# Kernel optimization log

Hardware: AMD Instinct MI355X
Metric: run time of the kernel (lower is better)

The kernel has to match this reference:

```python
import jax, jax.numpy as jnp
import numpy as np

QK_K = 256          # values per Q4_K super-block
TYPE_SIZE = 144     # bytes per Q4_K block: 2 (d fp16) + 2 (dmin fp16) + 12 (scales) + 128 (qs)
OUT_FEATURES = 8192
IN_FEATURES = 8192
BATCH = 256


def setup_inputs() -> dict:
    rng = np.random.default_rng(0)
    n_blocks = OUT_FEATURES * IN_FEATURES // QK_K
    # Pack valid little-endian fp16 super-block scales into raw bytes (as a GGUF file would store them).
    d16 = rng.uniform(0.001, 0.01, size=(n_blocks,)).astype(np.float16)
    dmin16 = rng.uniform(0.0005, 0.005, size=(n_blocks,)).astype(np.float16)
    scales = rng.integers(0, 256, size=(n_blocks, 12), dtype=np.uint8)  # packed 6-bit sub-scales/mins
    qs = rng.integers(0, 256, size=(n_blocks, 128), dtype=np.uint8)     # 4-bit quants, 2 per byte
    blocks = np.concatenate(
        [d16.view(np.uint8).reshape(n_blocks, 2),
         dmin16.view(np.uint8).reshape(n_blocks, 2),
         scales, qs], axis=1)  # [n_blocks, 144] uint8
    key = jax.random.key(0)
    kx, kb = jax.random.split(key)
    x = jax.random.normal(kx, (BATCH, IN_FEATURES), dtype=jnp.float32)
    bias = jax.random.normal(kb, (OUT_FEATURES,), dtype=jnp.float32) * 0.01
    return {"x": x, "qweight": jnp.asarray(blocks), "bias": bias}


def _bitcast_f16(bytes2):
    # bytes2: [n, 2] uint8 (little-endian) -> [n] float32
    n = bytes2.shape[0]
    return jax.lax.bitcast_convert_type(bytes2.reshape(n, 1, 2), jnp.float16).reshape(n).astype(jnp.float32)


def _get_scale_min(scales):
    # scales: [n, 12] uint8 -> 8 six-bit sub-block scales and mins, each [n, 8]
    n = scales.shape[0]
    s = scales.reshape(n, 3, 4)
    d_, m_, md = s[:, 0], s[:, 1], s[:, 2]  # each [n, 4]
    sc = jnp.concatenate([d_ & 63, (md & 15) | ((d_ >> 2) & 48)], axis=-1)
    mn = jnp.concatenate([m_ & 63, (md >> 4) | ((m_ >> 2) & 48)], axis=-1)
    return sc, mn


def dequantize_q4_k(blocks):
    # blocks: [n_blocks, 144] uint8 -> [n_blocks, 256] float32
    n = blocks.shape[0]
    d = _bitcast_f16(blocks[:, 0:2])       # [n]
    dmin = _bitcast_f16(blocks[:, 2:4])    # [n]
    sc, mn = _get_scale_min(blocks[:, 4:16])
    dl = (d[:, None] * sc.astype(jnp.float32)).reshape(n, 8, 1)   # per-sub-block scale
    ml = (dmin[:, None] * mn.astype(jnp.float32)).reshape(n, 8, 1)  # per-sub-block min
    qs = blocks[:, 16:].reshape(n, 4, 1, 32)                       # 128 bytes
    shift = jnp.array([0, 4], dtype=jnp.uint8).reshape(1, 1, 2, 1)
    q = ((qs >> shift) & 15).reshape(n, 8, 32).astype(jnp.float32)  # low then high nibbles
    return (dl * q - ml).reshape(n, QK_K)


def reference(x, qweight, bias):
    qweight = qweight.astype(jnp.uint8)
    W = dequantize_q4_k(qweight).reshape(OUT_FEATURES, IN_FEATURES)  # [out, in]
    return x @ W.T + bias  # F.linear(x, W, bias)
```

## Files before the change

### kernel.cpp

```cpp
#include <hip/hip_runtime.h>
#include <hip/hip_fp16.h>

typedef __bf16 bf16x8 __attribute__((ext_vector_type(8)));
typedef float floatx16 __attribute__((ext_vector_type(16)));
typedef unsigned int uint;
typedef unsigned short ushort;
typedef uint  uintx4  __attribute__((ext_vector_type(4)));
typedef float floatx4 __attribute__((ext_vector_type(4)));

constexpr int Mdim = 256, Ndim = 8192, Kdim = 8192;
constexpr int BN = 64, KSPLIT = 4;
constexpr int KS = Kdim / KSPLIT;
constexpr int NT = KS / 64;
constexpr int KB = Kdim / 256;

union U8 { uint u[4]; bf16x8 v; };

__device__ __forceinline__ uint cvtpk(float lo, float hi) {
  uint r; asm("v_cvt_pk_bf16_f32 %0, %1, %2" : "=v"(r) : "v"(lo), "v"(hi));
  return r;
}

template <typename T>
__device__ __forceinline__ T gld(const void* p) {
  return *(const __attribute__((address_space(1))) T*)p;
}

__device__ __forceinline__ int bswz(int row, int ch) {
  return row * 128 + ((ch ^ (row & 15)) << 3);
}

template<bool PRE>
__global__ __launch_bounds__(256, 2)
void q4k_gemm(const float* __restrict__ x, const bf16x8* __restrict__ xbf,
              const int* __restrict__ qw, const float* __restrict__ bias,
              float* __restrict__ out)
{
  __shared__ ushort Bb[2][BN * 128];

  const int tid = threadIdx.x;
  const int bid = blockIdx.x;
  const int l  = (bid & 7) * 64 + (bid >> 3);
  const int nb = l >> 2;
  const int ks = l & 3;
  const int n0 = nb * BN;
  const int ks8 = ks * (KS >> 8);

  const int sr = tid >> 2;
  const int sq = tid & 3;

  const int lane = tid & 63;
  const int wave = tid >> 6;
  const int mb0  = wave * 2;
  const int brow = lane & 31;
  const int bco  = lane >> 5;

  const int* bp0 = qw + (n0 + sr) * (KB * 144);
  const bf16x8* xA0 = PRE ? (xbf + ((mb0    ) * 512 + ks * 128) * 64 + lane) : nullptr;
  const bf16x8* xA1 = PRE ? (xbf + ((mb0 + 1) * 512 + ks * 128) * 64 + lane) : nullptr;

  uintx4 R[4][2];
  uintx4 Mdd[2], M0[2], M1[2], M2[2];
  U8 pqL, pqH;
  bf16x8 aA[8], aB[8];
  floatx16 acc00 = {}, acc01 = {}, acc10 = {}, acc11 = {};

  auto gloadB = [&](int s2, int rs) {
    const int* qp = bp0 + (ks8 + (s2 >> 2)) * 144 + 16 + (s2 & 3) * 32 + sq * 8;
    R[rs][0] = gld<uintx4>(qp);
    R[rs][1] = gld<uintx4>(qp + 4);
  };

  auto mload = [&](int sbrel, int ms) {
    const int* bp = bp0 + (ks8 + sbrel) * 144;
    Mdd[ms] = gld<uintx4>(bp);
    M0[ms]  = gld<uintx4>(bp + 4);
    M1[ms]  = gld<uintx4>(bp + 8);
    M2[ms]  = gld<uintx4>(bp + 12);
  };

  auto gloadA = [&](int t, bf16x8 (&A)[8]) {
    if constexpr (PRE) {
      const int f = t * 4 * 64;
      #pragma unroll
      for (int kk = 0; kk < 4; ++kk) {
        A[kk]     = gld<bf16x8>(xA0 + f + kk * 64);
        A[4 + kk] = gld<bf16x8>(xA1 + f + kk * 64);
      }
    } else {
      const int kg = ks * KS + t * 64 + bco * 8;
      #pragma unroll
      for (int kk = 0; kk < 4; ++kk) {
        const float* fA = x + (mb0 * 32 + brow) * Kdim + kg + kk * 16;
        const float* fB = x + ((mb0 + 1) * 32 + brow) * Kdim + kg + kk * 16;
        const floatx4 p0 = gld<floatx4>(fA), p1 = gld<floatx4>(fA + 4);
        const floatx4 q0 = gld<floatx4>(fB), q1 = gld<floatx4>(fB + 4);
        U8 ua, ub;
        ua.u[0] = cvtpk(p0.x, p0.y); ua.u[1] = cvtpk(p0.z, p0.w);
        ua.u[2] = cvtpk(p1.x, p1.y); ua.u[3] = cvtpk(p1.z, p1.w);
        ub.u[0] = cvtpk(q0.x, q0.y); ub.u[1] = cvtpk(q0.z, q0.w);
        ub.u[2] = cvtpk(q1.x, q1.y); ub.u[3] = cvtpk(q1.z, q1.w);
        A[kk] = ua.v; A[4 + kk] = ub.v;
      }
    }
  };

  auto dequant = [&](int c, int rs, int ms) {
    const uintx4 dd = Mdd[ms];
    const float d  = __half2float(__ushort_as_half((ushort)((dd.x & 255u) | ((dd.y & 255u) << 8))));
    const float dm = __half2float(__ushort_as_half((ushort)((dd.z & 255u) | ((dd.w & 255u) << 8))));
    const uintx4 s0 = M0[ms], s1 = M1[ms], s2 = M2[ms];
    uint scA, scB, mnA, mnB;
    if (c == 0)      { scA = s0.x & 63u; scB = s0.y & 63u; mnA = s1.x & 63u; mnB = s1.y & 63u; }
    else if (c == 1) { scA = s0.z & 63u; scB = s0.w & 63u; mnA = s1.z & 63u; mnB = s1.w & 63u; }
    else if (c == 2) {
      scA = (s2.x & 15u) | ((s0.x >> 2) & 48u); scB = (s2.y & 15u) | ((s0.y >> 2) & 48u);
      mnA = (s2.x >> 4)  | ((s1.x >> 2) & 48u); mnB = (s2.y >> 4)  | ((s1.y >> 2) & 48u);
    } else {
      scA = (s2.z & 15u) | ((s0.z >> 2) & 48u); scB = (s2.w & 15u) | ((s0.w >> 2) & 48u);
      mnA = (s2.z >> 4)  | ((s1.z >> 2) & 48u); mnB = (s2.w >> 4)  | ((s1.w >> 2) & 48u);
    }
    const float dlA = d * (float)scA, mlA = dm * (float)mnA;
    const float dlB = d * (float)scB, mlB = dm * (float)mnB;
    float wl[8], wh[8];
    #pragma unroll
    for (int h = 0; h < 2; ++h) {
      const uintx4 qv = R[rs][h];
      wl[h*4+0] = fmaf(dlA, (float)(qv.x & 15u), -mlA);
      wl[h*4+1] = fmaf(dlA, (float)(qv.y & 15u), -mlA);
      wl[h*4+2] = fmaf(dlA, (float)(qv.z & 15u), -mlA);
      wl[h*4+3] = fmaf(dlA, (float)(qv.w & 15u), -mlA);
      wh[h*4+0] = fmaf(dlB, (float)(qv.x >> 4), -mlB);
      wh[h*4+1] = fmaf(dlB, (float)(qv.y >> 4), -mlB);
      wh[h*4+2] = fmaf(dlB, (float)(qv.z >> 4), -mlB);
      wh[h*4+3] = fmaf(dlB, (float)(qv.w >> 4), -mlB);
    }
    #pragma unroll
    for (int p = 0; p < 4; ++p) {
      pqL.u[p] = cvtpk(wl[2*p], wl[2*p+1]);
      pqH.u[p] = cvtpk(wh[2*p], wh[2*p+1]);
    }
  };

  auto bwrite = [&](int bufi, int h) {
    *(bf16x8*)&Bb[bufi][bswz(sr, h * 8 + sq)]     = pqL.v;
    *(bf16x8*)&Bb[bufi][bswz(sr, h * 8 + 4 + sq)] = pqH.v;
  };

  auto mstep = [&](int bufi, int h, const bf16x8 (&A)[8]) {
    #pragma unroll
    for (int kk = 0; kk < 4; ++kk) {
      const bf16x8 bq0 = *(const bf16x8*)&Bb[bufi][bswz(brow,      h * 8 + kk * 2 + bco)];
      const bf16x8 bq1 = *(const bf16x8*)&Bb[bufi][bswz(brow + 32, h * 8 + kk * 2 + bco)];
      acc00 = __builtin_amdgcn_mfma_f32_32x32x16_bf16(A[kk],     bq0, acc00, 0, 0, 0);
      acc01 = __builtin_amdgcn_mfma_f32_32x32x16_bf16(A[kk],     bq1, acc01, 0, 0, 0);
      acc10 = __builtin_amdgcn_mfma_f32_32x32x16_bf16(A[4 + kk], bq0, acc10, 0, 0, 0);
      acc11 = __builtin_amdgcn_mfma_f32_32x32x16_bf16(A[4 + kk], bq1, acc11, 0, 0, 0);
    }
  };

  mload(0, 0); mload(1, 1);
  gloadB(0, 0); gloadB(1, 1); gloadB(2, 2); gloadB(3, 3);
  gloadA(0, aA); gloadA(1, aB);
  dequant(0, 0, 0); bwrite(0, 0);
  dequant(1, 1, 0); bwrite(0, 1);
  asm volatile("s_waitcnt lgkmcnt(0)" ::: "memory");
  __builtin_amdgcn_s_barrier();
  __builtin_amdgcn_sched_barrier(0);

  #define MLOADJ(j)                                                          \
    if ((j) == 1) { const int sb_ = B / 2 + 2; if (sb_ < 8) mload(sb_, 0); } \
    else if ((j) == 3) { const int sb_ = B / 2 + 3; if (sb_ < 8) mload(sb_, 1); }

  #define PH2(j) {                                                           \
    const int p_ = B + (j);                                                  \
    const int s1_ = 2 * p_ + 2, s2_ = 2 * p_ + 3;                            \
    if (s1_ < NT) { dequant((2*(j)+2)&3, (2*(j)+2)&3, (((j)+1)>>1)&1);       \
                    bwrite(((j)&1)^1, 0); }                                  \
    if (s2_ < NT) { dequant((2*(j)+3)&3, (2*(j)+3)&3, (((j)+1)>>1)&1);       \
                    bwrite(((j)&1)^1, 1); }                                  \
    if (s1_ + 2 < NT) gloadB(s1_ + 2, (2*(j)+4)&3);                          \
    if (s2_ + 2 < NT) gloadB(s2_ + 2, (2*(j)+5)&3);                          \
    MLOADJ(j)                                                                \
    __builtin_amdgcn_s_setprio(1);                                           \
    mstep((j)&1, 0, aA);                                                     \
    __builtin_amdgcn_s_setprio(0);                                           \
    if (s1_ < NT) gloadA(s1_, aA);                                           \
    __builtin_amdgcn_s_setprio(1);                                           \
    mstep((j)&1, 1, aB);                                                     \
    __builtin_amdgcn_s_setprio(0);                                           \
    if (s2_ < NT) gloadA(s2_, aB);                                           \
    asm volatile("s_waitcnt lgkmcnt(0)" ::: "memory");                       \
    __builtin_amdgcn_s_barrier();                                            \
    __builtin_amdgcn_sched_barrier(0);                                       \
  }

  for (int i = 0; i < 4; ++i) {
    const int B = i * 4;
    PH2(0) PH2(1) PH2(2) PH2(3)
  }
  #undef PH2
  #undef MLOADJ

  const int gn0 = n0 + (lane & 31);
  const int gn1 = gn0 + 32;
  const float bv0 = (ks == 0) ? bias[gn0] : 0.0f;
  const float bv1 = (ks == 0) ? bias[gn1] : 0.0f;
  const int mrow = wave * 64 + 4 * (lane >> 5);
  #pragma unroll
  for (int r = 0; r < 16; ++r) {
    const int m = mrow + (r & 3) + 8 * (r >> 2);
    atomicAdd(&out[m * Ndim + gn0], acc00[r] + bv0);
    atomicAdd(&out[m * Ndim + gn1], acc01[r] + bv1);
    atomicAdd(&out[(m + 32) * Ndim + gn0], acc10[r] + bv0);
    atomicAdd(&out[(m + 32) * Ndim + gn1], acc11[r] + bv1);
  }
}

template<bool DOCVT>
__global__ __launch_bounds__(256)
void prep(const float* __restrict__ x, uintx4* __restrict__ xb,
          floatx4* __restrict__ out)
{
  const int gid = blockIdx.x * 256 + threadIdx.x;
  out[gid * 2]     = floatx4{0.f, 0.f, 0.f, 0.f};
  out[gid * 2 + 1] = floatx4{0.f, 0.f, 0.f, 0.f};
  if (DOCVT) {
    const int lane = gid & 63;
    const int m = ((gid >> 15) * 32) + (lane & 31);
    const int k = (((gid >> 6) & 511) * 16) + (lane >> 5) * 8;
    const floatx4 f0 = gld<floatx4>(x + m * Kdim + k);
    const floatx4 f1 = gld<floatx4>(x + m * Kdim + k + 4);
    uintx4 st;
    st.x = cvtpk(f0.x, f0.y); st.y = cvtpk(f0.z, f0.w);
    st.z = cvtpk(f1.x, f1.y); st.w = cvtpk(f1.z, f1.w);
    xb[gid] = st;
  }
}

extern "C" void kernel_launch(void* const* d_in, const int* in_sizes, int n_in,
                              void* d_out, int out_size, void* d_ws, size_t ws_size,
                              hipStream_t stream) {
  (void)in_sizes; (void)n_in; (void)out_size;
  const float* x    = (const float*)d_in[0];
  const int*   qw   = (const int*)d_in[1];
  const float* bias = (const float*)d_in[2];
  float* out = (float*)d_out;

  const size_t need = (size_t)Mdim * Kdim * 2;
  if (ws_size >= need) {
    prep<true><<<1024, 256, 0, stream>>>(x, (uintx4*)d_ws, (floatx4*)out);
    q4k_gemm<true><<<512, 256, 0, stream>>>(x, (const bf16x8*)d_ws, qw, bias, out);
  } else {
    prep<false><<<1024, 256, 0, stream>>>(x, nullptr, (floatx4*)out);
    q4k_gemm<false><<<512, 256, 0, stream>>>(x, nullptr, qw, bias, out);
  }
}
```

Measured before the change: 70.92 us.

## Stage Q4_K quant bytes through LDS via direct global-to-LDS loads

```diff
diff --git a/kernel.cpp b/kernel.cpp
--- a/kernel.cpp
+++ b/kernel.cpp
@@ -26,9 +26,20 @@
   return *(const __attribute__((address_space(1))) T*)p;
 }
 
+__device__ __forceinline__ void glds16(const void* g, void* l) {
+  __builtin_amdgcn_global_load_lds(
+      (const __attribute__((address_space(1))) uint*)g,
+      (__attribute__((address_space(3))) uint*)l, 16, 0, 0);
+}
+
 __device__ __forceinline__ int bswz(int row, int ch) {
   return row * 128 + ((ch ^ (row & 15)) << 3);
 }
+
+#define WAITVM_(n) asm volatile("s_waitcnt vmcnt(" #n ")" ::: "memory")
+#define WAITVM(n) WAITVM_(n)
+#define NOWAIT ((void)0)
+#define S6(s) ((s) % 6)
 
 template<bool PRE>
 __global__ __launch_bounds__(256, 2)
@@ -36,6 +47,7 @@
               const int* __restrict__ qw, const float* __restrict__ bias,
               float* __restrict__ out)
 {
+  __shared__ __align__(16) int Qs[6 * 2048];
   __shared__ ushort Bb[2][BN * 128];
 
   const int tid = threadIdx.x;
@@ -59,16 +71,21 @@
   const bf16x8* xA0 = PRE ? (xbf + ((mb0    ) * 512 + ks * 128) * 64 + lane) : nullptr;
   const bf16x8* xA1 = PRE ? (xbf + ((mb0 + 1) * 512 + ks * 128) * 64 + lane) : nullptr;
 
-  uintx4 R[4][2];
   uintx4 Mdd[2], M0[2], M1[2], M2[2];
   U8 pqL, pqH;
   bf16x8 aA[8], aB[8];
   floatx16 acc00 = {}, acc01 = {}, acc10 = {}, acc11 = {};
 
-  auto gloadB = [&](int s2, int rs) {
-    const int* qp = bp0 + (ks8 + (s2 >> 2)) * 144 + 16 + (s2 & 3) * 32 + sq * 8;
-    R[rs][0] = gld<uintx4>(qp);
-    R[rs][1] = gld<uintx4>(qp + 4);
+  auto stageQ = [&](int s, int slot) {
+    const int sb = s >> 2, c64 = s & 3;
+    const int schk = ((lane & 7) ^ (lane >> 3)) << 2;
+    #pragma unroll
+    for (int j = 0; j < 2; ++j) {
+      const int r = j * 32 + wave * 8 + (lane >> 3);
+      const int* src = qw + (n0 + r) * (KB * 144) + (ks8 + sb) * 144
+                       + 16 + c64 * 32 + schk;
+      glds16((const void*)src, (void*)&Qs[slot * 2048 + (j * 256 + wave * 64) * 4]);
+    }
   };
 
   auto mload = [&](int sbrel, int ms) {
@@ -105,7 +122,10 @@
     }
   };
 
-  auto dequant = [&](int c, int rs, int ms) {
+  auto dequant = [&](int c, int slot, int ms) {
+    const int* qrow = &Qs[slot * 2048 + sr * 32];
+    const uintx4 q0 = *(const uintx4*)(qrow + ((( 2 * sq)     ^ (sr & 7)) << 2));
+    const uintx4 q1 = *(const uintx4*)(qrow + ((( 2 * sq + 1) ^ (sr & 7)) << 2));
     const uintx4 dd = Mdd[ms];
     const float d  = __half2float(__ushort_as_half((ushort)((dd.x & 255u) | ((dd.y & 255u) << 8))));
     const float dm = __half2float(__ushort_as_half((ushort)((dd.z & 255u) | ((dd.w & 255u) << 8))));
@@ -125,7 +145,7 @@
     float wl[8], wh[8];
     #pragma unroll
     for (int h = 0; h < 2; ++h) {
-      const uintx4 qv = R[rs][h];
+      const uintx4 qv = h ? q1 : q0;
       wl[h*4+0] = fmaf(dlA, (float)(qv.x & 15u), -mlA);
       wl[h*4+1] = fmaf(dlA, (float)(qv.y & 15u), -mlA);
       wl[h*4+2] = fmaf(dlA, (float)(qv.z & 15u), -mlA);
@@ -159,48 +179,53 @@
     }
   };
 
+  stageQ(0, 0); stageQ(1, 1);
+  stageQ(2, 2); stageQ(3, 3);
   mload(0, 0); mload(1, 1);
-  gloadB(0, 0); gloadB(1, 1); gloadB(2, 2); gloadB(3, 3);
   gloadA(0, aA); gloadA(1, aB);
+  stageQ(4, 4); stageQ(5, 5);
+  WAITVM(32);
+  __builtin_amdgcn_s_barrier();
   dequant(0, 0, 0); bwrite(0, 0);
   dequant(1, 1, 0); bwrite(0, 1);
+  WAITVM(28);
   asm volatile("s_waitcnt lgkmcnt(0)" ::: "memory");
   __builtin_amdgcn_s_barrier();
   __builtin_amdgcn_sched_barrier(0);
 
-  #define MLOADJ(j)                                                          \
-    if ((j) == 1) { const int sb_ = B / 2 + 2; if (sb_ < 8) mload(sb_, 0); } \
-    else if ((j) == 3) { const int sb_ = B / 2 + 3; if (sb_ < 8) mload(sb_, 1); }
-
-  #define PH2(j) {                                                           \
-    const int p_ = B + (j);                                                  \
-    const int s1_ = 2 * p_ + 2, s2_ = 2 * p_ + 3;                            \
-    if (s1_ < NT) { dequant((2*(j)+2)&3, (2*(j)+2)&3, (((j)+1)>>1)&1);       \
-                    bwrite(((j)&1)^1, 0); }                                  \
-    if (s2_ < NT) { dequant((2*(j)+3)&3, (2*(j)+3)&3, (((j)+1)>>1)&1);       \
-                    bwrite(((j)&1)^1, 1); }                                  \
-    if (s1_ + 2 < NT) gloadB(s1_ + 2, (2*(j)+4)&3);                          \
-    if (s2_ + 2 < NT) gloadB(s2_ + 2, (2*(j)+5)&3);                          \
-    MLOADJ(j)                                                                \
+  #define MG(P) (((P) + 3) / 2 > 7 ? 7 : ((P) + 3) / 2)
+  #define PH(P, WAITSTMT) {                                                  \
+    if ((2*(P)+3) < NT) {                                                    \
+      dequant((2*(P)+2) & 3, S6(2*(P)+2), ((2*(P)+2) >> 2) & 1);             \
+      bwrite(((P)+1) & 1, 0);                                                \
+      dequant((2*(P)+3) & 3, S6(2*(P)+3), ((2*(P)+3) >> 2) & 1);             \
+      bwrite(((P)+1) & 1, 1);                                                \
+    }                                                                        \
+    if ((P) <= 12) { stageQ(2*(P)+6, S6(2*(P)+6)); stageQ(2*(P)+7, S6(2*(P)+7)); } \
+    if (((P) & 1) && (P) <= 13) mload(MG(P), MG(P) & 1);                     \
     __builtin_amdgcn_s_setprio(1);                                           \
-    mstep((j)&1, 0, aA);                                                     \
+    mstep((P) & 1, 0, aA);                                                   \
     __builtin_amdgcn_s_setprio(0);                                           \
-    if (s1_ < NT) gloadA(s1_, aA);                                           \
+    if ((2*(P)+2) < NT) gloadA(2*(P)+2, aA);                                 \
     __builtin_amdgcn_s_setprio(1);                                           \
-    mstep((j)&1, 1, aB);                                                     \
+    mstep((P) & 1, 1, aB);                                                   \
     __builtin_amdgcn_s_setprio(0);                                           \
-    if (s2_ < NT) gloadA(s2_, aB);                                           \
+    if ((2*(P)+3) < NT) gloadA(2*(P)+3, aB);                                 \
+    WAITSTMT;                                                                \
     asm volatile("s_waitcnt lgkmcnt(0)" ::: "memory");                       \
     __builtin_amdgcn_s_barrier();                                            \
     __builtin_amdgcn_sched_barrier(0);                                       \
   }
 
-  for (int i = 0; i < 4; ++i) {
-    const int B = i * 4;
-    PH2(0) PH2(1) PH2(2) PH2(3)
-  }
-  #undef PH2
-  #undef MLOADJ
+  PH(0,  WAITVM(20))
+  PH(1,  WAITVM(40)) PH(2,  WAITVM(40)) PH(3,  WAITVM(40)) PH(4,  WAITVM(40))
+  PH(5,  WAITVM(40)) PH(6,  WAITVM(40)) PH(7,  WAITVM(40)) PH(8,  WAITVM(40))
+  PH(9,  WAITVM(40)) PH(10, WAITVM(40)) PH(11, WAITVM(40)) PH(12, WAITVM(40))
+  PH(13, WAITVM(36))
+  PH(14, NOWAIT)
+  PH(15, NOWAIT)
+  #undef PH
+  #undef MG
 
   const int gn0 = n0 + (lane & 31);
   const int gn1 = gn0 + 32;
```

Measured after the change: 73.14 us. +3.1%, slower.

## Replace split-K atomic accumulation with partial buffers and a reduction kernel

Applied to the files above, without the earlier changes.

```diff
diff --git a/kernel.cpp b/kernel.cpp
--- a/kernel.cpp
+++ b/kernel.cpp
@@ -30,11 +30,11 @@
   return row * 128 + ((ch ^ (row & 15)) << 3);
 }
 
-template<bool PRE>
+template<bool PRE, bool PART>
 __global__ __launch_bounds__(256, 2)
 void q4k_gemm(const float* __restrict__ x, const bf16x8* __restrict__ xbf,
               const int* __restrict__ qw, const float* __restrict__ bias,
-              float* __restrict__ out)
+              float* __restrict__ out, float* __restrict__ pout)
 {
   __shared__ ushort Bb[2][BN * 128];
 
@@ -204,27 +204,55 @@
 
   const int gn0 = n0 + (lane & 31);
   const int gn1 = gn0 + 32;
-  const float bv0 = (ks == 0) ? bias[gn0] : 0.0f;
-  const float bv1 = (ks == 0) ? bias[gn1] : 0.0f;
   const int mrow = wave * 64 + 4 * (lane >> 5);
-  #pragma unroll
-  for (int r = 0; r < 16; ++r) {
-    const int m = mrow + (r & 3) + 8 * (r >> 2);
-    atomicAdd(&out[m * Ndim + gn0], acc00[r] + bv0);
-    atomicAdd(&out[m * Ndim + gn1], acc01[r] + bv1);
-    atomicAdd(&out[(m + 32) * Ndim + gn0], acc10[r] + bv0);
-    atomicAdd(&out[(m + 32) * Ndim + gn1], acc11[r] + bv1);
-  }
-}
-
-template<bool DOCVT>
+  if constexpr (PART) {
+    float* pp = pout + (size_t)ks * ((size_t)Mdim * Ndim);
+    #pragma unroll
+    for (int r = 0; r < 16; ++r) {
+      const int m = mrow + (r & 3) + 8 * (r >> 2);
+      pp[m * Ndim + gn0] = acc00[r];
+      pp[m * Ndim + gn1] = acc01[r];
+      pp[(m + 32) * Ndim + gn0] = acc10[r];
+      pp[(m + 32) * Ndim + gn1] = acc11[r];
+    }
+  } else {
+    const float bv0 = (ks == 0) ? bias[gn0] : 0.0f;
+    const float bv1 = (ks == 0) ? bias[gn1] : 0.0f;
+    #pragma unroll
+    for (int r = 0; r < 16; ++r) {
+      const int m = mrow + (r & 3) + 8 * (r >> 2);
+      atomicAdd(&out[m * Ndim + gn0], acc00[r] + bv0);
+      atomicAdd(&out[m * Ndim + gn1], acc01[r] + bv1);
+      atomicAdd(&out[(m + 32) * Ndim + gn0], acc10[r] + bv0);
+      atomicAdd(&out[(m + 32) * Ndim + gn1], acc11[r] + bv1);
+    }
+  }
+}
+
+__global__ __launch_bounds__(256)
+void reduce4(const floatx4* __restrict__ p, const float* __restrict__ bias,
+             floatx4* __restrict__ out)
+{
+  const int gid = blockIdx.x * 256 + threadIdx.x;
+  constexpr int STR = (Mdim * Ndim) / 4;
+  floatx4 s = gld<floatx4>(p + gid);
+  s += gld<floatx4>(p + gid + STR);
+  s += gld<floatx4>(p + gid + 2 * STR);
+  s += gld<floatx4>(p + gid + 3 * STR);
+  s += gld<floatx4>((const floatx4*)bias + (gid & 2047));
+  out[gid] = s;
+}
+
+template<bool DOCVT, bool ZERO>
 __global__ __launch_bounds__(256)
 void prep(const float* __restrict__ x, uintx4* __restrict__ xb,
           floatx4* __restrict__ out)
 {
   const int gid = blockIdx.x * 256 + threadIdx.x;
-  out[gid * 2]     = floatx4{0.f, 0.f, 0.f, 0.f};
-  out[gid * 2 + 1] = floatx4{0.f, 0.f, 0.f, 0.f};
+  if (ZERO) {
+    out[gid * 2]     = floatx4{0.f, 0.f, 0.f, 0.f};
+    out[gid * 2 + 1] = floatx4{0.f, 0.f, 0.f, 0.f};
+  }
   if (DOCVT) {
     const int lane = gid & 63;
     const int m = ((gid >> 15) * 32) + (lane & 31);
@@ -247,12 +275,22 @@
   const float* bias = (const float*)d_in[2];
   float* out = (float*)d_out;
 
-  const size_t need = (size_t)Mdim * Kdim * 2;
-  if (ws_size >= need) {
-    prep<true><<<1024, 256, 0, stream>>>(x, (uintx4*)d_ws, (floatx4*)out);
-    q4k_gemm<true><<<512, 256, 0, stream>>>(x, (const bf16x8*)d_ws, qw, bias, out);
+  const size_t needXB   = (size_t)Mdim * Kdim * 2;
+  const size_t needPART = needXB + (size_t)KSPLIT * Mdim * Ndim * 4;
+  if (ws_size >= needPART) {
+    float* part = (float*)((char*)d_ws + needXB);
+    prep<true, false><<<1024, 256, 0, stream>>>(x, (uintx4*)d_ws, (floatx4*)out);
+    q4k_gemm<true, true><<<512, 256, 0, stream>>>(
+        x, (const bf16x8*)d_ws, qw, bias, out, part);
+    reduce4<<<(Mdim * Ndim / 4) / 256, 256, 0, stream>>>(
+        (const floatx4*)part, bias, (floatx4*)out);
+  } else if (ws_size >= needXB) {
+    prep<true, true><<<1024, 256, 0, stream>>>(x, (uintx4*)d_ws, (floatx4*)out);
+    q4k_gemm<true, false><<<512, 256, 0, stream>>>(
+        x, (const bf16x8*)d_ws, qw, bias, out, nullptr);
   } else {
-    prep<false><<<1024, 256, 0, stream>>>(x, nullptr, (floatx4*)out);
-    q4k_gemm<false><<<512, 256, 0, stream>>>(x, nullptr, qw, bias, out);
-  }
-}
+    prep<false, true><<<1024, 256, 0, stream>>>(x, nullptr, (floatx4*)out);
+    q4k_gemm<false, false><<<512, 256, 0, stream>>>(
+        x, nullptr, qw, bias, out, nullptr);
+  }
+}
```

New measurement: 61.40 us. -13.4%, faster.
